# Kernel tuning notes

Measured on AMD Instinct MI355X. Metric: run time of the kernel, lower is better.

Reference implementation:

```python
import jax, jax.numpy as jnp
import numpy as np
from jax import lax

BATCH = 512
FS = 24        # filter_size
QDIM = 11      # sort-of-clevr question vector length
IMG = 80       # 80 -> 40 -> 20 -> 10 -> 5 via four stride-2 convs
D = 5
OBJ = D * D    # 25 objects
PAIR_IN = (FS + 2) * 2 + QDIM  # 63
HID = 256
EPS = 1e-5


def setup_inputs() -> dict:
    key = jax.random.key(0)
    ks = jax.random.split(key, 24)

    def n(k, shape, s=0.05):
        return jax.random.normal(k, shape, jnp.float32) * s

    inp = {
        "img": jax.random.normal(ks[0], (BATCH, 3, IMG, IMG), jnp.float32),
        "qst": jax.random.normal(ks[1], (QDIM, BATCH), jnp.float32),
    }
    chans = [3, FS, FS, FS]
    ki = 2
    for l in range(4):
        inp[f"cw{l+1}"] = n(ks[ki], (FS, chans[l], 3, 3)); ki += 1
        inp[f"cb{l+1}"] = jnp.zeros((FS,), jnp.float32)
        inp[f"bg{l+1}"] = jnp.ones((FS,), jnp.float32)
        inp[f"bb{l+1}"] = jnp.zeros((FS,), jnp.float32)
    g_in = [PAIR_IN, HID, HID, HID]
    for l in range(4):
        inp[f"g{l+1}w"] = n(ks[ki], (HID, g_in[l])); ki += 1
        inp[f"g{l+1}b"] = jnp.zeros((HID,), jnp.float32)
    inp["f1w"] = n(ks[ki], (HID, HID)); ki += 1
    inp["f1b"] = jnp.zeros((HID,), jnp.float32)
    inp["fc2w"] = n(ks[ki], (HID, HID)); ki += 1
    inp["fc2b"] = jnp.zeros((HID,), jnp.float32)
    inp["fc3w"] = n(ks[ki], (10, HID)); ki += 1
    inp["fc3b"] = jnp.zeros((10,), jnp.float32)
    return inp


def _conv_bn(x, w, b, gamma, beta):
    # conv stride 2, pad 1 -> relu -> batchnorm (training-mode batch stats)
    y = lax.conv_general_dilated(x, w, (2, 2), [(1, 1), (1, 1)],
                                 dimension_numbers=("NCHW", "OIHW", "NCHW"))
    y = jax.nn.relu(y + b[None, :, None, None])
    mean = y.mean(axis=(0, 2, 3))
    var = y.var(axis=(0, 2, 3))
    inv = gamma * lax.rsqrt(var + EPS)
    return (y - mean[None, :, None, None]) * inv[None, :, None, None] + beta[None, :, None, None]


def _lin(x, w, b):
    return x @ w.T + b


def reference(img, qst,
              cw1, cb1, bg1, bb1, cw2, cb2, bg2, bb2,
              cw3, cb3, bg3, bb3, cw4, cb4, bg4, bb4,
              g1w, g1b, g2w, g2b, g3w, g3b, g4w, g4b,
              f1w, f1b, fc2w, fc2b, fc3w, fc3b):
    q = qst.T  # [mb, QDIM] (torch.transpose(qst,0,1).float())

    x = _conv_bn(img, cw1, cb1, bg1, bb1)
    x = _conv_bn(x, cw2, cb2, bg2, bb2)
    x = _conv_bn(x, cw3, cb3, bg3, bb3)
    x = _conv_bn(x, cw4, cb4, bg4, bb4)   # [mb, FS, 5, 5]

    mb = x.shape[0]
    x_flat = x.reshape(mb, FS, OBJ).transpose(0, 2, 1)  # [mb, 25, FS]

    idx = jnp.arange(OBJ)
    coord = jnp.stack([(idx // 5 - 2) / 2.0, (idx % 5 - 2) / 2.0], axis=-1).astype(jnp.float32)
    x_flat = jnp.concatenate([x_flat, jnp.broadcast_to(coord, (mb, OBJ, 2))], axis=2)  # [mb,25,FS+2]

    # pair[b, k, i] = concat(obj_i, obj_k, q)  (matches torch x_i/x_j/cat layout)
    oi = jnp.broadcast_to(x_flat[:, None, :, :], (mb, OBJ, OBJ, FS + 2))
    oj = jnp.broadcast_to(x_flat[:, :, None, :], (mb, OBJ, OBJ, FS + 2))
    qq = jnp.broadcast_to(q[:, None, None, :], (mb, OBJ, OBJ, QDIM))
    pairs = jnp.concatenate([oi, oj, qq], axis=3).reshape(mb * OBJ * OBJ, PAIR_IN)

    h = jax.nn.relu(_lin(pairs, g1w, g1b))
    h = jax.nn.relu(_lin(h, g2w, g2b))
    h = jax.nn.relu(_lin(h, g3w, g3b))
    h = jax.nn.relu(_lin(h, g4w, g4b))
    x_g = h.reshape(mb, OBJ * OBJ, HID).sum(axis=1)  # [mb, 256]

    x_f = jax.nn.relu(_lin(x_g, f1w, f1b))
    x_f = jax.nn.relu(_lin(x_f, fc2w, fc2b))
    # dropout treated as identity (eval-mode deterministic reference)
    logits = _lin(x_f, fc3w, fc3b)
    return jax.nn.log_softmax(logits, axis=-1)
```

## Files before the change

### kernel.cpp

```cpp
#include <hip/hip_runtime.h>
#include <math.h>

#define MB    512
#define FS    24
#define QDIM  11
#define OBJ   25
#define HID   256

typedef unsigned short u16;
typedef __attribute__((ext_vector_type(8))) __bf16 bf16x8;
typedef __attribute__((ext_vector_type(4))) __bf16 bf16x4;
typedef __attribute__((ext_vector_type(4))) float f32x4;
typedef __attribute__((ext_vector_type(8))) float f32x8;

__device__ __forceinline__ float bf2f(u16 h) {
    return __uint_as_float(((unsigned int)h) << 16);
}
__device__ __forceinline__ u16 f2bf(float f) {
    unsigned int u = __float_as_uint(f);
    return (u16)((u + 0x7FFFu + ((u >> 16) & 1u)) >> 16);
}

__global__ __launch_bounds__(256) void prep_all(
    const float* __restrict__ g2w, const float* __restrict__ g3w,
    const float* __restrict__ g4w, u16* __restrict__ wfrag,
    const float* __restrict__ cw1, const float* __restrict__ cw2,
    const float* __restrict__ cw3, const float* __restrict__ cw4,
    float* __restrict__ wt1, u16* __restrict__ wcfrag)
{
    if (blockIdx.x < 768) {
        int idx = blockIdx.x * 256 + threadIdx.x;
        int jj = idx & 7;
        int lane = (idx >> 3) & 63;
        int tn = (idx >> 9) & 15;
        int c = (idx >> 13) & 7;
        int l = idx >> 16;
        const float* W = (l == 0) ? g2w : ((l == 1) ? g3w : g4w);
        int n = tn * 16 + (lane & 15);
        int k = c * 32 + (lane >> 4) * 8 + jj;
        wfrag[idx] = f2bf(W[n * 256 + k]);
    } else {
        int idx = (blockIdx.x - 768) * 256 + threadIdx.x;
        if (idx < 648) {
            int k = idx / 24, oc = idx % 24;
            wt1[idx] = cw1[oc * 27 + k];
        } else if (idx < 648 + 27648) {
            int t = idx - 648;
            int l = t / 9216, r = t % 9216;
            int cell = r / 1024, rr = r % 1024;
            int o = rr / 512, q = rr % 512;
            int lane = q / 8, j = q % 8;
            int oc = o * 16 + (lane & 15);
            int ic = (lane >> 4) * 8 + j;
            const float* w = (l == 0) ? cw2 : ((l == 1) ? cw3 : cw4);
            u16 v = 0;
            if (oc < 24 && ic < 24) v = f2bf(w[oc * 216 + ic * 9 + cell]);
            wcfrag[t] = v;
        }
    }
}

__global__ __launch_bounds__(256) void conv1_t(
    const float* __restrict__ img, const float* __restrict__ wt1,
    const float* __restrict__ bias, float* __restrict__ yout,
    float* __restrict__ stats)
{
    __shared__ float tile[3 * 21 * 85];
    __shared__ float part[48];
    const int tid = threadIdx.x;
    const int b   = blockIdx.x >> 2;
    const int y0  = (blockIdx.x & 3) * 10;
    const int iy_base = 2 * y0 - 1;
    for (int e = tid; e < 3 * 21 * 85; e += 256) {
        int ixt = e % 85; int rem = e / 85;
        int iyl = rem % 21; int ic = rem / 21;
        int iy = iy_base + iyl, ix = ixt - 1;
        float v = 0.f;
        if ((unsigned)iy < 80u && (unsigned)ix < 80u)
            v = img[((size_t)(b * 3 + ic) * 80 + iy) * 80 + ix];
        tile[e] = v;
    }
    if (tid < 48) part[tid] = 0.f;
    __syncthreads();

    float rsum[24], rsq[24];
#pragma unroll
    for (int oc = 0; oc < 24; oc++) { rsum[oc] = 0.f; rsq[oc] = 0.f; }

#pragma unroll 1
    for (int pp = 0; pp < 2; pp++) {
        const int pxl = tid + pp * 256;
        const bool active = pxl < 400;
        const int pxc = active ? pxl : 0;
        const int yl = pxc / 40, x = pxc % 40;
        float acc[24];
#pragma unroll
        for (int oc = 0; oc < 24; oc++) acc[oc] = bias[oc];
#pragma unroll 1
        for (int ic = 0; ic < 3; ic++) {
#pragma unroll 1
            for (int ky = 0; ky < 3; ky++) {
#pragma unroll 1
                for (int kx = 0; kx < 3; kx++) {
                    const int k = (ic * 3 + ky) * 3 + kx;
                    float xin = tile[ic * 1785 + (2 * yl + ky) * 85 + (2 * x + kx)];
                    const float4* wrow = (const float4*)&wt1[k * 24];
#pragma unroll
                    for (int g = 0; g < 6; g++) {
                        float4 wv = wrow[g];
                        acc[g * 4 + 0] = fmaf(xin, wv.x, acc[g * 4 + 0]);
                        acc[g * 4 + 1] = fmaf(xin, wv.y, acc[g * 4 + 1]);
                        acc[g * 4 + 2] = fmaf(xin, wv.z, acc[g * 4 + 2]);
                        acc[g * 4 + 3] = fmaf(xin, wv.w, acc[g * 4 + 3]);
                    }
                }
            }
        }
#pragma unroll
        for (int oc = 0; oc < 24; oc++)
            acc[oc] = active ? fmaxf(acc[oc], 0.f) : 0.f;
        if (active) {
            float* op = &yout[((size_t)b * 1600 + (y0 + yl) * 40 + x) * 24];
#pragma unroll
            for (int g = 0; g < 6; g++)
                *(float4*)&op[g * 4] = make_float4(acc[g * 4], acc[g * 4 + 1],
                                                   acc[g * 4 + 2], acc[g * 4 + 3]);
        }
#pragma unroll
        for (int oc = 0; oc < 24; oc++) {
            rsum[oc] += acc[oc];
            rsq[oc]  += acc[oc] * acc[oc];
        }
    }

    {
        float v[48];
#pragma unroll
        for (int oc = 0; oc < 24; oc++) { v[oc] = rsum[oc]; v[24 + oc] = rsq[oc]; }
        const int ln = tid & 63;
#pragma unroll
        for (int i = 0; i < 48; i++) v[i] += __shfl_xor(v[i], 1, 64);
        {
            const bool bs = (ln & 1) != 0;
#pragma unroll
            for (int i = 0; i < 24; i++) v[i] = bs ? v[24 + i] : v[i];
        }
#pragma unroll
        for (int i = 0; i < 24; i++) v[i] += __shfl_xor(v[i], 2, 64);
        {
            const bool bs = (ln & 2) != 0;
#pragma unroll
            for (int i = 0; i < 12; i++) v[i] = bs ? v[12 + i] : v[i];
        }
#pragma unroll
        for (int i = 0; i < 12; i++) v[i] += __shfl_xor(v[i], 4, 64);
        {
            const bool bs = (ln & 4) != 0;
#pragma unroll
            for (int i = 0; i < 6; i++) v[i] = bs ? v[6 + i] : v[i];
        }
#pragma unroll
        for (int i = 0; i < 6; i++) v[i] += __shfl_xor(v[i], 8, 64);
        {
            const bool bs = (ln & 8) != 0;
#pragma unroll
            for (int i = 0; i < 3; i++) v[i] = bs ? v[3 + i] : v[i];
        }
#pragma unroll
        for (int i = 0; i < 3; i++) {
            v[i] += __shfl_xor(v[i], 16, 64);
            v[i] += __shfl_xor(v[i], 32, 64);
        }
        if (ln < 16) {
            const int base = (ln & 1) * 24 + ((ln >> 1) & 1) * 12
                           + ((ln >> 2) & 1) * 6 + ((ln >> 3) & 1) * 3;
#pragma unroll
            for (int i = 0; i < 3; i++) atomicAdd(&part[base + i], v[i]);
        }
    }
    __syncthreads();
    if (tid < 48) atomicAdd(&stats[tid], part[tid]);
}

template<int HIN, int HOUT, int YT, int MT>
__global__ __launch_bounds__(256) void convM(
    const float* __restrict__ yin,
    const float* __restrict__ stp, const float* __restrict__ gam,
    const float* __restrict__ bet, float invN,
    const u16* __restrict__ wcf_g,
    const float* __restrict__ bias,
    float* __restrict__ yout, float* __restrict__ stats)
{
    constexpr int ROWS = 2 * YT + 1;
    constexpr int R    = 2 * HOUT + 1;
    constexpr int POS  = ROWS * R;
    constexpr int NPX  = HOUT * HOUT;
    constexpr int NPXB = YT * HOUT;
    constexpr int TILES = HOUT / YT;
    constexpr int MTPW = (MT + 3) / 4;
    __shared__ __align__(16) u16 tile[POS * 24 + 16];
    __shared__ float scW[48];
    __shared__ float part[48];
    const int tid  = threadIdx.x;
    const int b    = (TILES == 1) ? blockIdx.x : (int)(blockIdx.x / TILES);
    const int y0   = (TILES == 1) ? 0 : (int)(blockIdx.x % TILES) * YT;
    const int lane = tid & 63, wave = tid >> 6;
    const int r16  = lane & 15, quad = lane >> 4;

    if (tid < 24) {
        float m   = stp[tid] * invN;
        float var = stp[24 + tid] * invN - m * m;
        float inv = gam[tid] * rsqrtf(var + 1e-5f);
        scW[tid]      = inv;
        scW[24 + tid] = bet[tid] - m * inv;
    }
    if (tid < 48) part[tid] = 0.f;

    bf16x8 wcf[9][2];
#pragma unroll
    for (int c = 0; c < 9; c++)
#pragma unroll
        for (int o = 0; o < 2; o++)
            wcf[c][o] = *(const bf16x8*)&wcf_g[((c * 2 + o) * 64 + lane) * 8];

    __syncthreads();

    f32x8 scv[3], ofv[3];
#pragma unroll
    for (int g = 0; g < 3; g++)
#pragma unroll
        for (int c2 = 0; c2 < 8; c2++) {
            scv[g][c2] = scW[g * 8 + c2];
            ofv[g][c2] = scW[24 + g * 8 + c2];
        }

    const int iy_base = 2 * y0 - 1;
    for (int p = tid; p < POS; p += 256) {
        int iyl = p / R, ixt = p % R;
        int iy = iy_base + iyl, ix = ixt - 1;
        if ((unsigned)iy < (unsigned)HIN && (unsigned)ix < (unsigned)HIN) {
            const float4* ip4 = (const float4*)&yin[((size_t)b * HIN * HIN + iy * HIN + ix) * 24];
#pragma unroll
            for (int g = 0; g < 3; g++) {
                float4 A = ip4[g * 2], B = ip4[g * 2 + 1];
                f32x8 xv = {A.x, A.y, A.z, A.w, B.x, B.y, B.z, B.w};
                f32x8 r = xv * scv[g] + ofv[g];
                bf16x8 hb = __builtin_convertvector(r, bf16x8);
                *(uint4*)&tile[p * 24 + g * 8] = *(uint4*)&hb;
            }
        } else {
            uint4 z = make_uint4(0, 0, 0, 0);
#pragma unroll
            for (int g = 0; g < 3; g++)
                *(uint4*)&tile[p * 24 + g * 8] = z;
        }
    }
    __syncthreads();

    f32x4 acc[MTPW][2];
#pragma unroll
    for (int t = 0; t < MTPW; t++) {
        acc[t][0] = (f32x4)(0.f);
        acc[t][1] = (f32x4)(0.f);
    }

    int baseT[MTPW];
#pragma unroll
    for (int t = 0; t < MTPW; t++) {
        int mt = wave + t * 4;
        int pxl = mt * 16 + r16;
        if (pxl > NPXB - 1) pxl = NPXB - 1;
        baseT[t] = ((2 * (pxl / HOUT)) * R + 2 * (pxl % HOUT)) * 24 + quad * 8;
    }

#pragma unroll
    for (int ky = 0; ky < 3; ky++) {
#pragma unroll
        for (int kx = 0; kx < 3; kx++) {
            const int cell = ky * 3 + kx;
            const int coff = (ky * R + kx) * 24;
            bf16x8 xf[MTPW];
#pragma unroll
            for (int t = 0; t < MTPW; t++) {
                int mt = wave + t * 4;
                uint4 tmp = make_uint4(0, 0, 0, 0);
                if (mt < MT && quad < 3)
                    tmp = *(const uint4*)&tile[baseT[t] + coff];
                xf[t] = *(bf16x8*)&tmp;
            }
#pragma unroll
            for (int t = 0; t < MTPW; t++) {
                int mt = wave + t * 4;
                if (mt < MT) {
                    acc[t][0] = __builtin_amdgcn_mfma_f32_16x16x32_bf16(
                        wcf[cell][0], xf[t], acc[t][0], 0, 0, 0);
                    acc[t][1] = __builtin_amdgcn_mfma_f32_16x16x32_bf16(
                        wcf[cell][1], xf[t], acc[t][1], 0, 0, 0);
                }
            }
        }
    }

    float ss[2][4], qq[2][4];
#pragma unroll
    for (int o = 0; o < 2; o++)
#pragma unroll
        for (int r = 0; r < 4; r++) { ss[o][r] = 0.f; qq[o][r] = 0.f; }

#pragma unroll
    for (int t = 0; t < MTPW; t++) {
        int mt = wave + t * 4;
        if (mt >= MT) continue;
        int pxl = mt * 16 + r16;
        bool pv = pxl < NPXB;
        int pxi = y0 * HOUT + pxl;
#pragma unroll
        for (int o = 0; o < 2; o++) {
            int ocb = o * 16 + quad * 4;
            if (pv && ocb < 24) {
                float4 bb = *(const float4*)&bias[ocb];
                float v0 = fmaxf(acc[t][o][0] + bb.x, 0.f);
                float v1 = fmaxf(acc[t][o][1] + bb.y, 0.f);
                float v2 = fmaxf(acc[t][o][2] + bb.z, 0.f);
                float v3 = fmaxf(acc[t][o][3] + bb.w, 0.f);
                *(float4*)&yout[((size_t)b * NPX + pxi) * 24 + ocb] =
                    make_float4(v0, v1, v2, v3);
                ss[o][0] += v0; qq[o][0] += v0 * v0;
                ss[o][1] += v1; qq[o][1] += v1 * v1;
                ss[o][2] += v2; qq[o][2] += v2 * v2;
                ss[o][3] += v3; qq[o][3] += v3 * v3;
            }
        }
    }
#pragma unroll
    for (int o = 0; o < 2; o++) {
        int ocb = o * 16 + quad * 4;
#pragma unroll
        for (int r = 0; r < 4; r++) {
            float a = ss[o][r], q = qq[o][r];
            a += __shfl_xor(a, 1, 64); q += __shfl_xor(q, 1, 64);
            a += __shfl_xor(a, 2, 64); q += __shfl_xor(q, 2, 64);
            a += __shfl_xor(a, 4, 64); q += __shfl_xor(q, 4, 64);
            a += __shfl_xor(a, 8, 64); q += __shfl_xor(q, 8, 64);
            if (r16 == 0 && ocb < 24) {
                atomicAdd(&part[ocb + r], a);
                atomicAdd(&part[24 + ocb + r], q);
            }
        }
    }
    __syncthreads();
    if (tid < 48) atomicAdd(&stats[tid], part[tid]);
}

__global__ __launch_bounds__(256) void uv_kernel(
    const float* __restrict__ y4t,
    const float* __restrict__ stp, const float* __restrict__ gam,
    const float* __restrict__ bet, float invN,
    const float* __restrict__ qst, const float* __restrict__ g1w,
    const float* __restrict__ g1b, u16* __restrict__ u, u16* __restrict__ v)
{
    int b = blockIdx.x, tid = threadIdx.x;
    __shared__ float xf[650];
    __shared__ float qv[11];
    __shared__ float scW[48];
    if (tid < 24) {
        float m   = stp[tid] * invN;
        float var = stp[24 + tid] * invN - m * m;
        float inv = gam[tid] * rsqrtf(var + 1e-5f);
        scW[tid]      = inv;
        scW[24 + tid] = bet[tid] - m * inv;
    }
    __syncthreads();
    for (int e = tid; e < 650; e += 256) {
        int o = e / 26, c = e % 26;
        float val;
        if (c < 24)      val = y4t[b * 600 + o * 24 + c] * scW[c] + scW[24 + c];
        else if (c == 24) val = (float)(o / 5 - 2) * 0.5f;
        else              val = (float)(o % 5 - 2) * 0.5f;
        xf[e] = val;
    }
    if (tid < 11) qv[tid] = qst[tid * MB + b];
    __syncthreads();
    const int n = tid;
    float wrow[63];
#pragma unroll
    for (int c = 0; c < 63; c++) wrow[c] = g1w[n * 63 + c];
    float qsum = g1b[n];
#pragma unroll
    for (int j = 0; j < 11; j++) qsum += wrow[52 + j] * qv[j];
    for (int o = 0; o < 25; o++) {
        float uu = 0.f, vv = qsum;
#pragma unroll
        for (int c = 0; c < 26; c++) {
            uu += wrow[c]      * xf[o * 26 + c];
            vv += wrow[26 + c] * xf[o * 26 + c];
        }
        u[(b * 25 + o) * 256 + n] = f2bf(uu);
        v[(b * 25 + o) * 256 + n] = f2bf(vv);
    }
}

__global__ __launch_bounds__(256, 2) void g_fused(
    const u16* __restrict__ u_bf, const u16* __restrict__ v_bf,
    const u16* __restrict__ wfrag,
    const float* __restrict__ b2, const float* __restrict__ b3, const float* __restrict__ b4,
    float* __restrict__ xg)
{
    __shared__ u16 hS[32768];
    const int tid  = threadIdx.x;
    const int b    = blockIdx.x / 5;
    const int p0   = (blockIdx.x % 5) * 128;
    const int lane = tid & 63, wave = tid >> 6;
    const int r16  = lane & 15, sub = lane >> 4;
    const int n0w  = wave * 64;

    const u16* wfL = wfrag + (size_t)(wave * 4) * 512 + (size_t)lane * 8;

    bf16x8 wcur[4], wnxt[4];
#pragma unroll
    for (int tn = 0; tn < 4; tn++)
        wcur[tn] = *(const bf16x8*)&wfL[(size_t)tn * 512];
#pragma unroll
    for (int tn = 0; tn < 4; tn++) wnxt[tn] = wcur[tn];

    {
        const int m = tid & 127, half = tid >> 7;
        const int p = p0 + m;
        if (p < 625) {
            const int oi = p % 25, ok = p / 25;
            const uint4* up = (const uint4*)(u_bf + (size_t)(b * 25 + oi) * 256);
            const uint4* vp = (const uint4*)(v_bf + (size_t)(b * 25 + ok) * 256);
#pragma unroll
            for (int gi = 0; gi < 16; gi++) {
                const int g = half * 16 + gi;
                uint4 ua = up[g], va = vp[g];
                bf16x8 ub = *(bf16x8*)&ua;
                bf16x8 vb = *(bf16x8*)&va;
                f32x8 uf = __builtin_convertvector(ub, f32x8);
                f32x8 vf = __builtin_convertvector(vb, f32x8);
                f32x8 hf = uf + vf;
                hf = __builtin_elementwise_max(hf, (f32x8)(0.f));
                bf16x8 hb = __builtin_convertvector(hf, bf16x8);
                *(uint4*)&hS[m * 256 + ((g ^ (m & 7)) * 8)] = *(uint4*)&hb;
            }
        } else {
            uint4 z = make_uint4(0, 0, 0, 0);
#pragma unroll
            for (int gi = 0; gi < 16; gi++) {
                const int g = half * 16 + gi;
                *(uint4*)&hS[m * 256 + ((g ^ (m & 7)) * 8)] = z;
            }
        }
    }

#pragma unroll 1
    for (int l = 0; l < 3; l++) {
        f32x4 acc[8][4];
#pragma unroll
        for (int tm = 0; tm < 8; tm++)
#pragma unroll
            for (int tn = 0; tn < 4; tn++)
                acc[tm][tn] = (f32x4)(0.f);

        __syncthreads();

#pragma unroll 1
        for (int kb = 0; kb < 8; kb++) {
            const int s = l * 8 + kb;
            if (s < 23) {
#pragma unroll
                for (int tn = 0; tn < 4; tn++)
                    wnxt[tn] = *(const bf16x8*)&wfL[((size_t)(s + 1) * 16 + tn) * 512];
            }
            bf16x8 bfr[8];
            const int g = kb * 4 + sub;
#pragma unroll
            for (int tm = 0; tm < 8; tm++) {
                const int m = tm * 16 + r16;
                bfr[tm] = *(const bf16x8*)&hS[m * 256 + ((g ^ (m & 7)) * 8)];
            }
#pragma unroll
            for (int tm = 0; tm < 8; tm++)
#pragma unroll
                for (int tn = 0; tn < 4; tn++)
                    acc[tm][tn] = __builtin_amdgcn_mfma_f32_16x16x32_bf16(
                        wcur[tn], bfr[tm], acc[tm][tn], 0, 0, 0);
#pragma unroll
            for (int tn = 0; tn < 4; tn++) wcur[tn] = wnxt[tn];
        }
        __syncthreads();

        const float* bl = (l == 0) ? b2 : ((l == 1) ? b3 : b4);
        if (l < 2) {
#pragma unroll
            for (int tn = 0; tn < 4; tn++) {
                const int n0 = n0w + tn * 16 + sub * 4;
                const float4 bb = *(const float4*)&bl[n0];
                const f32x4 bb4 = {bb.x, bb.y, bb.z, bb.w};
                const int gg = n0 >> 3;
                const int sh = (sub & 1) * 4;
#pragma unroll
                for (int tm = 0; tm < 8; tm++) {
                    const int m = tm * 16 + r16;
                    f32x4 t = acc[tm][tn] + bb4;
                    t = __builtin_elementwise_max(t, (f32x4)(0.f));
                    bf16x4 hb = __builtin_convertvector(t, bf16x4);
                    *(ushort4*)&hS[m * 256 + ((gg ^ (m & 7)) * 8) + sh] = *(ushort4*)&hb;
                }
            }
        } else {
            f32x4 sv[4];
#pragma unroll
            for (int tn = 0; tn < 4; tn++) sv[tn] = (f32x4)(0.f);
#pragma unroll
            for (int tn = 0; tn < 4; tn++) {
                const int n0 = n0w + tn * 16 + sub * 4;
                const float4 bb = *(const float4*)&bl[n0];
                const f32x4 bb4 = {bb.x, bb.y, bb.z, bb.w};
#pragma unroll
                for (int tm = 0; tm < 8; tm++) {
                    const int m = tm * 16 + r16;
                    if (p0 + m < 625) {
                        f32x4 t = acc[tm][tn] + bb4;
                        t = __builtin_elementwise_max(t, (f32x4)(0.f));
                        sv[tn] += t;
                    }
                }
            }
#pragma unroll
            for (int tn = 0; tn < 4; tn++)
#pragma unroll
                for (int r = 0; r < 4; r++) {
                    float v = sv[tn][r];
                    v += __shfl_xor(v, 1, 64);
                    v += __shfl_xor(v, 2, 64);
                    v += __shfl_xor(v, 4, 64);
                    v += __shfl_xor(v, 8, 64);
                    if (r16 == 0)
                        atomicAdd(&xg[b * 256 + n0w + tn * 16 + sub * 4 + r], v);
                }
        }
    }
}

__global__ __launch_bounds__(256) void f_fused(
    const float* __restrict__ xg,
    const float* __restrict__ f1w, const float* __restrict__ f1b,
    const float* __restrict__ fc2w, const float* __restrict__ fc2b,
    const float* __restrict__ fc3w, const float* __restrict__ fc3b,
    float* __restrict__ out)
{
    const int b = blockIdx.x, tid = threadIdx.x;
    __shared__ float xa[256], xb[256], lg[10], red[2];
    xa[tid] = xg[b * 256 + tid];
    __syncthreads();
    {
        const float4* wr = (const float4*)(f1w + (size_t)tid * 256);
        float a = f1b[tid];
#pragma unroll
        for (int k4 = 0; k4 < 64; k4++) {
            float4 w4 = wr[k4];
            a += w4.x * xa[k4 * 4 + 0] + w4.y * xa[k4 * 4 + 1]
               + w4.z * xa[k4 * 4 + 2] + w4.w * xa[k4 * 4 + 3];
        }
        xb[tid] = a > 0.f ? a : 0.f;
    }
    __syncthreads();
    {
        const float4* wr = (const float4*)(fc2w + (size_t)tid * 256);
        float a = fc2b[tid];
#pragma unroll
        for (int k4 = 0; k4 < 64; k4++) {
            float4 w4 = wr[k4];
            a += w4.x * xb[k4 * 4 + 0] + w4.y * xb[k4 * 4 + 1]
               + w4.z * xb[k4 * 4 + 2] + w4.w * xb[k4 * 4 + 3];
        }
        __syncthreads();
        xa[tid] = a > 0.f ? a : 0.f;
    }
    __syncthreads();
    if (tid < 10) {
        const float4* wr = (const float4*)(fc3w + (size_t)tid * 256);
        float a = fc3b[tid];
#pragma unroll
        for (int k4 = 0; k4 < 64; k4++) {
            float4 w4 = wr[k4];
            a += w4.x * xa[k4 * 4 + 0] + w4.y * xa[k4 * 4 + 1]
               + w4.z * xa[k4 * 4 + 2] + w4.w * xa[k4 * 4 + 3];
        }
        lg[tid] = a;
    }
    __syncthreads();
    if (tid == 0) {
        float mx = lg[0];
        for (int o = 1; o < 10; o++) mx = lg[o] > mx ? lg[o] : mx;
        float ssum = 0.f;
        for (int o = 0; o < 10; o++) ssum += expf(lg[o] - mx);
        red[0] = mx;
        red[1] = logf(ssum);
    }
    __syncthreads();
    if (tid < 10) out[b * 10 + tid] = lg[tid] - red[0] - red[1];
}

extern "C" void kernel_launch(void* const* d_in, const int* in_sizes, int n_in,
                              void* d_out, int out_size, void* d_ws, size_t ws_size,
                              hipStream_t stream)
{
    const float* img  = (const float*)d_in[0];
    const float* qst  = (const float*)d_in[1];
    const float* cw1  = (const float*)d_in[2];
    const float* cb1  = (const float*)d_in[3];
    const float* bg1  = (const float*)d_in[4];
    const float* bb1  = (const float*)d_in[5];
    const float* cw2  = (const float*)d_in[6];
    const float* cb2  = (const float*)d_in[7];
    const float* bg2  = (const float*)d_in[8];
    const float* bb2  = (const float*)d_in[9];
    const float* cw3  = (const float*)d_in[10];
    const float* cb3  = (const float*)d_in[11];
    const float* bg3  = (const float*)d_in[12];
    const float* bb3  = (const float*)d_in[13];
    const float* cw4  = (const float*)d_in[14];
    const float* cb4  = (const float*)d_in[15];
    const float* bg4  = (const float*)d_in[16];
    const float* bb4  = (const float*)d_in[17];
    const float* g1w  = (const float*)d_in[18];
    const float* g1b  = (const float*)d_in[19];
    const float* g2w  = (const float*)d_in[20];
    const float* g2b  = (const float*)d_in[21];
    const float* g3w  = (const float*)d_in[22];
    const float* g3b  = (const float*)d_in[23];
    const float* g4w  = (const float*)d_in[24];
    const float* g4b  = (const float*)d_in[25];
    const float* f1w  = (const float*)d_in[26];
    const float* f1b  = (const float*)d_in[27];
    const float* fc2w = (const float*)d_in[28];
    const float* fc2b = (const float*)d_in[29];
    const float* fc3w = (const float*)d_in[30];
    const float* fc3b = (const float*)d_in[31];
    float* out = (float*)d_out;

    float* ws    = (float*)d_ws;
    float* stats = ws;
    float* xg    = ws + 192;
    u16*   wfrag = (u16*)(ws + 131456);
    float* y1    = ws + 328064;
    float* y2    = ws + 19988864;
    float* y3    = ws + 24904064;
    float* y4    = ws + 26132864;
    u16*   u_bf  = (u16*)(ws + 26440064);
    u16*   v_bf  = (u16*)(ws + 28078464);
    float* wt1   = ws + 29716864;
    u16*   wcfrag = (u16*)(ws + 29717512);

    hipMemsetAsync(stats, 0, (size_t)131264 * sizeof(float), stream);

    prep_all<<<879, 256, 0, stream>>>(g2w, g3w, g4w, wfrag,
                                      cw1, cw2, cw3, cw4, wt1, wcfrag);

    conv1_t<<<2048, 256, 0, stream>>>(img, wt1, cb1, y1, stats);

    convM<40, 20, 4, 5><<<2560, 256, 0, stream>>>(
        y1, stats, bg1, bb1, 1.f / 819200.f, wcfrag, cb2, y2, stats + 48);
    convM<20, 10, 10, 7><<<512, 256, 0, stream>>>(
        y2, stats + 48, bg2, bb2, 1.f / 204800.f, wcfrag + 9216, cb3, y3, stats + 96);
    convM<10, 5, 5, 2><<<512, 256, 0, stream>>>(
        y3, stats + 96, bg3, bb3, 1.f / 51200.f, wcfrag + 18432, cb4, y4, stats + 144);

    uv_kernel<<<512, 256, 0, stream>>>(y4, stats + 144, bg4, bb4, 1.f / 12800.f,
                                       qst, g1w, g1b, u_bf, v_bf);

    g_fused<<<2560, 256, 0, stream>>>(u_bf, v_bf, wfrag, g2b, g3b, g4b, xg);

    f_fused<<<512, 256, 0, stream>>>(xg, f1w, f1b, fc2w, fc2b, fc3w, fc3b, out);
}
```

Measured before the change: 464.8 us.

## Fuse conv3, conv4 and uv stages into one persistent kernel with grid barriers

Merges the conv3, conv4 and uv kernels into a single 512-block kernel that uses device-wide atomic-counter barriers between stages. Batchnorm stat reads become atomic loads so each stage sees the previous stage's accumulated stats. The goal is to remove two kernel launch gaps and tail drain periods. The barrier relies on all 512 blocks being co-resident, and spin-waiting adds its own cost.

```diff
diff --git a/kernel.cpp b/kernel.cpp
--- a/kernel.cpp
+++ b/kernel.cpp
@@ -19,6 +19,23 @@
 __device__ __forceinline__ u16 f2bf(float f) {
     unsigned int u = __float_as_uint(f);
     return (u16)((u + 0x7FFFu + ((u >> 16) & 1u)) >> 16);
+}
+
+__device__ __forceinline__ float stat_ld(const float* p) {
+    return __hip_atomic_load(p, __ATOMIC_RELAXED, __HIP_MEMORY_SCOPE_AGENT);
+}
+
+__device__ __forceinline__ void dev_barrier(unsigned* ctr, unsigned n) {
+    __syncthreads();
+    __threadfence();
+    if (threadIdx.x == 0) {
+        __hip_atomic_fetch_add(ctr, 1u, __ATOMIC_ACQ_REL, __HIP_MEMORY_SCOPE_AGENT);
+        while (__hip_atomic_load(ctr, __ATOMIC_ACQUIRE, __HIP_MEMORY_SCOPE_AGENT) < n) {
+            __builtin_amdgcn_s_sleep(16);
+        }
+    }
+    __syncthreads();
+    __threadfence();
 }
 
 __global__ __launch_bounds__(256) void prep_all(
@@ -183,33 +200,31 @@
 }
 
 template<int HIN, int HOUT, int YT, int MT>
-__global__ __launch_bounds__(256) void convM(
+__device__ __forceinline__ void convM_body(
+    u16* tile, float* scW, float* part,
     const float* __restrict__ yin,
     const float* __restrict__ stp, const float* __restrict__ gam,
     const float* __restrict__ bet, float invN,
     const u16* __restrict__ wcf_g,
     const float* __restrict__ bias,
-    float* __restrict__ yout, float* __restrict__ stats)
-{
+    float* __restrict__ yout, float* __restrict__ stats,
+    int b, int y0)
+{
+    constexpr int R    = 2 * HOUT + 1;
     constexpr int ROWS = 2 * YT + 1;
-    constexpr int R    = 2 * HOUT + 1;
     constexpr int POS  = ROWS * R;
     constexpr int NPX  = HOUT * HOUT;
     constexpr int NPXB = YT * HOUT;
-    constexpr int TILES = HOUT / YT;
     constexpr int MTPW = (MT + 3) / 4;
-    __shared__ __align__(16) u16 tile[POS * 24 + 16];
-    __shared__ float scW[48];
-    __shared__ float part[48];
     const int tid  = threadIdx.x;
-    const int b    = (TILES == 1) ? blockIdx.x : (int)(blockIdx.x / TILES);
-    const int y0   = (TILES == 1) ? 0 : (int)(blockIdx.x % TILES) * YT;
     const int lane = tid & 63, wave = tid >> 6;
     const int r16  = lane & 15, quad = lane >> 4;
 
     if (tid < 24) {
-        float m   = stp[tid] * invN;
-        float var = stp[24 + tid] * invN - m * m;
+        float s0 = stat_ld(&stp[tid]);
+        float s1 = stat_ld(&stp[24 + tid]);
+        float m   = s0 * invN;
+        float var = s1 * invN - m * m;
         float inv = gam[tid] * rsqrtf(var + 1e-5f);
         scW[tid]      = inv;
         scW[24 + tid] = bet[tid] - m * inv;
@@ -352,20 +367,41 @@
     if (tid < 48) atomicAdd(&stats[tid], part[tid]);
 }
 
-__global__ __launch_bounds__(256) void uv_kernel(
+template<int HIN, int HOUT, int YT, int MT>
+__global__ __launch_bounds__(256) void convM(
+    const float* __restrict__ yin,
+    const float* __restrict__ stp, const float* __restrict__ gam,
+    const float* __restrict__ bet, float invN,
+    const u16* __restrict__ wcf_g,
+    const float* __restrict__ bias,
+    float* __restrict__ yout, float* __restrict__ stats)
+{
+    constexpr int POS = (2 * YT + 1) * (2 * HOUT + 1);
+    constexpr int TILES = HOUT / YT;
+    __shared__ __align__(16) u16 tile[POS * 24 + 16];
+    __shared__ float scW[48];
+    __shared__ float part[48];
+    const int b  = (TILES == 1) ? blockIdx.x : (int)(blockIdx.x / TILES);
+    const int y0 = (TILES == 1) ? 0 : (int)(blockIdx.x % TILES) * YT;
+    convM_body<HIN, HOUT, YT, MT>(tile, scW, part, yin, stp, gam, bet, invN,
+                                  wcf_g, bias, yout, stats, b, y0);
+}
+
+__device__ __forceinline__ void uv_body(
+    float* xf, float* qv, float* scW,
     const float* __restrict__ y4t,
     const float* __restrict__ stp, const float* __restrict__ gam,
     const float* __restrict__ bet, float invN,
     const float* __restrict__ qst, const float* __restrict__ g1w,
-    const float* __restrict__ g1b, u16* __restrict__ u, u16* __restrict__ v)
-{
-    int b = blockIdx.x, tid = threadIdx.x;
-    __shared__ float xf[650];
-    __shared__ float qv[11];
-    __shared__ float scW[48];
+    const float* __restrict__ g1b, u16* __restrict__ u, u16* __restrict__ v,
+    int b)
+{
+    const int tid = threadIdx.x;
     if (tid < 24) {
-        float m   = stp[tid] * invN;
-        float var = stp[24 + tid] * invN - m * m;
+        float s0 = stat_ld(&stp[tid]);
+        float s1 = stat_ld(&stp[24 + tid]);
+        float m   = s0 * invN;
+        float var = s1 * invN - m * m;
         float inv = gam[tid] * rsqrtf(var + 1e-5f);
         scW[tid]      = inv;
         scW[24 + tid] = bet[tid] - m * inv;
@@ -398,6 +434,35 @@
         u[(b * 25 + o) * 256 + n] = f2bf(uu);
         v[(b * 25 + o) * 256 + n] = f2bf(vv);
     }
+}
+
+__global__ __launch_bounds__(256) void tail_fused(
+    const float* __restrict__ y2, float* __restrict__ y3, float* __restrict__ y4,
+    float* __restrict__ stats, unsigned* __restrict__ bar,
+    const float* __restrict__ bg2, const float* __restrict__ bb2,
+    const float* __restrict__ bg3, const float* __restrict__ bb3,
+    const float* __restrict__ bg4, const float* __restrict__ bb4,
+    const u16* __restrict__ wcfrag,
+    const float* __restrict__ cb3, const float* __restrict__ cb4,
+    const float* __restrict__ qst, const float* __restrict__ g1w,
+    const float* __restrict__ g1b, u16* __restrict__ u, u16* __restrict__ v)
+{
+    __shared__ __align__(16) unsigned char smem[21248];
+    __shared__ float scW[48];
+    __shared__ float part[48];
+    const int b = blockIdx.x;
+
+    convM_body<20, 10, 10, 7>((u16*)smem, scW, part,
+                              y2, stats + 48, bg2, bb2, 1.f / 204800.f,
+                              wcfrag + 9216, cb3, y3, stats + 96, b, 0);
+    dev_barrier(&bar[0], 512);
+    convM_body<10, 5, 5, 2>((u16*)smem, scW, part,
+                            y3, stats + 96, bg3, bb3, 1.f / 51200.f,
+                            wcfrag + 18432, cb4, y4, stats + 144, b, 0);
+    dev_barrier(&bar[1], 512);
+    uv_body((float*)smem, (float*)smem + 2600, scW,
+            y4, stats + 144, bg4, bb4, 1.f / 12800.f,
+            qst, g1w, g1b, u, v, b);
 }
 
 __global__ __launch_bounds__(256, 2) void g_fused(
@@ -644,6 +709,7 @@
     float* ws    = (float*)d_ws;
     float* stats = ws;
     float* xg    = ws + 192;
+    unsigned* bar = (unsigned*)(ws + 131264);
     u16*   wfrag = (u16*)(ws + 131456);
     float* y1    = ws + 328064;
     float* y2    = ws + 19988864;
@@ -654,7 +720,7 @@
     float* wt1   = ws + 29716864;
     u16*   wcfrag = (u16*)(ws + 29717512);
 
-    hipMemsetAsync(stats, 0, (size_t)131264 * sizeof(float), stream);
+    hipMemsetAsync(stats, 0, (size_t)131328 * sizeof(float), stream);
 
     prep_all<<<879, 256, 0, stream>>>(g2w, g3w, g4w, wfrag,
                                       cw1, cw2, cw3, cw4, wt1, wcfrag);
@@ -663,13 +729,11 @@
 
     convM<40, 20, 4, 5><<<2560, 256, 0, stream>>>(
         y1, stats, bg1, bb1, 1.f / 819200.f, wcfrag, cb2, y2, stats + 48);
-    convM<20, 10, 10, 7><<<512, 256, 0, stream>>>(
-        y2, stats + 48, bg2, bb2, 1.f / 204800.f, wcfrag + 9216, cb3, y3, stats + 96);
-    convM<10, 5, 5, 2><<<512, 256, 0, stream>>>(
-        y3, stats + 96, bg3, bb3, 1.f / 51200.f, wcfrag + 18432, cb4, y4, stats + 144);
-
-    uv_kernel<<<512, 256, 0, stream>>>(y4, stats + 144, bg4, bb4, 1.f / 12800.f,
-                                       qst, g1w, g1b, u_bf, v_bf);
+
+    tail_fused<<<512, 256, 0, stream>>>(
+        y2, y3, y4, stats, bar,
+        bg2, bb2, bg3, bb3, bg4, bb4,
+        wcfrag, cb3, cb4, qst, g1w, g1b, u_bf, v_bf);
 
     g_fused<<<2560, 256, 0, stream>>>(u_bf, v_bf, wfrag, g2b, g3b, g4b, xg);
 
```

After: 617.7 us. +32.9%, slower.
